# Optimization experiments

Hardware: AMD Instinct MI355X
Metric: run time of the kernel (lower is better)

Reference implementation:

```python
import jax, jax.numpy as jnp
from jax import lax
import numpy as np

B, N, C, P = 8, 512, 256, 7
CQ = C // 4
NMS_THRESH = 0.5
BBOX_XFORM_CLIP = 4.135166556742356  # log(1000/16)


def setup_inputs():
    key = jax.random.key(0)
    ks = jax.random.split(key, 24)
    rn = lambda k, s, sc=0.02: jax.random.normal(k, s, jnp.float32) * sc
    box_feats_q = jax.random.normal(ks[0], (B, N, C, P, P), jnp.float32)
    box_feats_s = jax.random.normal(ks[1], (B, 1, C, P, P), jnp.float32)
    xy = jax.random.uniform(ks[2], (B, N, 2), jnp.float32, 0.0, 700.0)
    wh = jax.random.uniform(ks[3], (B, N, 2), jnp.float32, 8.0, 96.0)
    proposals = jnp.concatenate([xy, xy + wh], axis=-1)  # [B,N,4] valid x1y1x2y2
    image_size = jnp.array([800, 800], jnp.int32)  # (H, W)
    return {
        'box_feats_q': box_feats_q, 'box_feats_s': box_feats_s,
        'proposals': proposals, 'image_size': image_size,
        'W1': rn(ks[4], (CQ, 2 * C)),          # conv1 1x1: 2C -> C/4
        'W2': rn(ks[5], (CQ, CQ, 3, 3)),       # conv2 3x3 valid
        'W3': rn(ks[6], (C, CQ)),              # conv3 1x1: C/4 -> C
        'Wcor': rn(ks[7], (C, C)),             # conv_cor 1x1
        'fc1_w': rn(ks[8], (C, 2 * C)), 'fc1_b': jnp.zeros((C,), jnp.float32),
        'fc2_w': rn(ks[9], (C, C)), 'fc2_b': jnp.zeros((C,), jnp.float32),
        'sfc_w': rn(ks[10], (1, C)), 'sfc_b': jnp.zeros((1,), jnp.float32),
        'scor_w': rn(ks[11], (1, C)), 'scor_b': jnp.zeros((1,), jnp.float32),
        'spr_w': rn(ks[12], (1, C)), 'spr_b': jnp.zeros((1,), jnp.float32),
        'dpr_w': rn(ks[13], (4, C)), 'dpr_b': jnp.zeros((4,), jnp.float32),
    }


def avgpool3(x):  # AvgPool2d(3, stride=1), NCHW
    s = lax.reduce_window(x, 0.0, lax.add, (1, 1, 3, 3), (1, 1, 1, 1), 'VALID')
    return s / 9.0


def head_forward(box_feats_q, box_feats_s, W1, W2, W3, Wcor, fc1_w, fc1_b, fc2_w,
                 fc2_b, sfc_w, sfc_b, scor_w, scor_b, spr_w, spr_b, dpr_w, dpr_b):
    M = B * N
    x_q = box_feats_q.reshape(M, C, P, P)
    x_s = jnp.broadcast_to(box_feats_s, (B, N, C, P, P)).reshape(M, C, P, P)
    # FC branch (avgpool_fc == global mean over 7x7)
    x_fc = jnp.concatenate([x_q.mean((2, 3)), x_s.mean((2, 3))], axis=1)  # [M,2C]
    h = jax.nn.relu(x_fc @ fc1_w.T + fc1_b)
    h = jax.nn.relu(h @ fc2_w.T + fc2_b)
    score_fc = h @ sfc_w.T + sfc_b  # [M,1]
    # Correlation branch: grouped 7x7 conv == per-channel spatial dot product
    x_cor_q = jnp.einsum('oc,mchw->mohw', Wcor, x_q)
    x_cor_s = jnp.einsum('oc,mchw->mohw', Wcor, x_s)
    x_relu = jax.nn.relu((x_cor_q * x_cor_s).sum((2, 3)))  # [M,C]
    score_cor = x_relu @ scor_w.T + scor_b  # [M,1]
    # Conv branch
    x = jnp.concatenate([x_q, x_s], axis=1)                    # [M,2C,7,7]
    x = jax.nn.relu(jnp.einsum('oc,mchw->mohw', W1, x))        # [M,CQ,7,7]
    x = avgpool3(x)                                            # [M,CQ,5,5]
    x = jax.nn.relu(lax.conv_general_dilated(x, W2, (1, 1), 'VALID',
        dimension_numbers=('NCHW', 'OIHW', 'NCHW')))           # [M,CQ,3,3]
    x = jax.nn.relu(jnp.einsum('oc,mchw->mohw', W3, x))        # [M,C,3,3]
    x = avgpool3(x).squeeze(3).squeeze(2)                      # [M,C]
    score_pr = x @ spr_w.T + spr_b
    pred_scores = score_pr + score_cor + score_fc              # [M,1]
    pred_deltas = x @ dpr_w.T + dpr_b                          # [M,4]
    return pred_scores, pred_deltas


def decode_boxes(deltas, boxes):
    w = boxes[:, 2] - boxes[:, 0]
    h = boxes[:, 3] - boxes[:, 1]
    cx = boxes[:, 0] + 0.5 * w
    cy = boxes[:, 1] + 0.5 * h
    dx, dy = deltas[:, 0], deltas[:, 1]
    dw = jnp.minimum(deltas[:, 2], BBOX_XFORM_CLIP)
    dh = jnp.minimum(deltas[:, 3], BBOX_XFORM_CLIP)
    pcx, pcy = dx * w + cx, dy * h + cy
    pw, ph = jnp.exp(dw) * w, jnp.exp(dh) * h
    return jnp.stack([pcx - 0.5 * pw, pcy - 0.5 * ph,
                      pcx + 0.5 * pw, pcy + 0.5 * ph], axis=1)


def nms_mask(boxes, scores, thresh):  # fixed-shape NMS -> keep mask [n]
    n = boxes.shape[0]
    order = jnp.argsort(-scores)
    b = boxes[order]
    area = jnp.maximum(b[:, 2] - b[:, 0], 0) * jnp.maximum(b[:, 3] - b[:, 1], 0)
    idx = jnp.arange(n)

    def body(i, keep):
        x1 = jnp.maximum(b[i, 0], b[:, 0]); y1 = jnp.maximum(b[i, 1], b[:, 1])
        x2 = jnp.minimum(b[i, 2], b[:, 2]); y2 = jnp.minimum(b[i, 3], b[:, 3])
        inter = jnp.maximum(x2 - x1, 0) * jnp.maximum(y2 - y1, 0)
        iou = inter / jnp.maximum(area[i] + area - inter, 1e-9)
        suppress = (iou > thresh) & (idx > i) & keep[i]
        return keep & ~suppress

    keep_sorted = lax.fori_loop(0, n, body, jnp.ones((n,), bool))
    return jnp.zeros((n,), bool).at[order].set(keep_sorted)


def reference(box_feats_q, box_feats_s, proposals, image_size, W1, W2, W3, Wcor,
              fc1_w, fc1_b, fc2_w, fc2_b, sfc_w, sfc_b, scor_w, scor_b,
              spr_w, spr_b, dpr_w, dpr_b):
    pred_scores, pred_deltas = head_forward(
        box_feats_q, box_feats_s, W1, W2, W3, Wcor, fc1_w, fc1_b, fc2_w, fc2_b,
        sfc_w, sfc_b, scor_w, scor_b, spr_w, spr_b, dpr_w, dpr_b)
    M = B * N
    # decode on detached deltas
    pred_boxes = decode_boxes(lax.stop_gradient(pred_deltas), proposals.reshape(M, 4))
    H = image_size[0].astype(jnp.float32)
    W_ = image_size[1].astype(jnp.float32)
    pred_boxes = jnp.stack([
        jnp.clip(pred_boxes[:, 0], 0.0, W_), jnp.clip(pred_boxes[:, 1], 0.0, H),
        jnp.clip(pred_boxes[:, 2], 0.0, W_), jnp.clip(pred_boxes[:, 3], 0.0, H)],
        axis=1).reshape(B, N, 4)
    scores = jax.nn.sigmoid(lax.stop_gradient(pred_scores)).reshape(B, N)
    keep = jax.vmap(lambda bx, sc: nms_mask(bx, sc, NMS_THRESH))(pred_boxes, scores)
    # boxes/scores padded to fixed [B,N,...]; keep mask marks NMS survivors
    return pred_boxes, scores, keep
```

## Files before the change

### kernel.cpp

```cpp
#include <hip/hip_runtime.h>
#include <math.h>

typedef float f4 __attribute__((ext_vector_type(4)));
typedef f4 f4u __attribute__((aligned(4)));
typedef float f32x4 __attribute__((ext_vector_type(4)));
typedef short short8 __attribute__((ext_vector_type(8)));

constexpr int NB  = 8;
constexpr int NN  = 512;
constexpr int NC  = 256;
constexpr int NHW = 49;
constexpr int NM  = NB * NN;
constexpr int XS  = 260;

constexpr size_t WS_SMEAN = 0;
constexpr size_t WS_YST   = 2048;
constexpr size_t WS_UST   = 102400;
constexpr size_t WS_WFH   = 127488;
constexpr size_t WS_WFL   = 168448;
constexpr size_t WS_SP    = 209408;
constexpr size_t WS_QMEAN = 213504;
constexpr size_t WS_SBOX  = WS_QMEAN;
constexpr size_t WS_SAREA = WS_SBOX + 16384;
constexpr size_t WS_SIDX  = WS_SAREA + 4096;
constexpr size_t WS_MASK  = WS_SIDX + 4096;

constexpr size_t OUT_SCORES = (size_t)NM * 4;
constexpr size_t OUT_KEEP   = OUT_SCORES + NM;

__device__ __forceinline__ float block_reduce_sum(float v, float* red) {
    int t = threadIdx.x;
#pragma unroll
    for (int off = 32; off > 0; off >>= 1) v += __shfl_down(v, off, 64);
    __syncthreads();
    if ((t & 63) == 0) red[t >> 6] = v;
    __syncthreads();
    return red[0] + red[1] + red[2] + red[3];
}

__device__ __forceinline__ unsigned short bf16_rne(float f) {
    unsigned u = __float_as_uint(f);
    return (unsigned short)((u + 0x7FFFu + ((u >> 16) & 1u)) >> 16);
}
__device__ __forceinline__ float bf16_to_f(unsigned short h) {
    return __uint_as_float(((unsigned)h) << 16);
}

__device__ __forceinline__ void stage_xT(const float* __restrict__ g, float* sx, int t) {
#pragma unroll
    for (int rep = 0; rep < 13; ++rep) {
        int id = rep * 256 + t;
        if (id < 3136) {
            int c4 = id / 49;
            int hw = id - c4 * 49;
            f4 v;
            v[0] = g[(c4 * 4 + 0) * 49 + hw];
            v[1] = g[(c4 * 4 + 1) * 49 + hw];
            v[2] = g[(c4 * 4 + 2) * 49 + hw];
            v[3] = g[(c4 * 4 + 3) * 49 + hw];
            *(f4*)&sx[hw * XS + c4 * 4] = v;
        }
    }
}

__global__ __launch_bounds__(64) void k_wfrag(
    const float* __restrict__ Wcor, const float* __restrict__ W1,
    float* __restrict__ ws)
{
    int l = threadIdx.x, blk = blockIdx.x;
    int mt = blk >> 3, ks = blk & 7;
    int row = mt * 16 + (l & 15);
    int k0 = ks * 32 + (l >> 4) * 8;
    const float* src = (row < 256) ? (Wcor + (size_t)row * 256 + k0)
                                   : (W1 + (size_t)(row - 256) * 512 + k0);
    short hv[8], lv[8];
#pragma unroll
    for (int j = 0; j < 8; ++j) {
        float v = src[j];
        unsigned short hh = bf16_rne(v);
        unsigned short hl = bf16_rne(v - bf16_to_f(hh));
        hv[j] = (short)hh; lv[j] = (short)hl;
    }
    short* dh = (short*)(ws + WS_WFH) + ((size_t)blk * 64 + l) * 8;
    short* dl = (short*)(ws + WS_WFL) + ((size_t)blk * 64 + l) * 8;
#pragma unroll
    for (int j = 0; j < 8; ++j) { dh[j] = hv[j]; dl[j] = lv[j]; }
}

__global__ __launch_bounds__(256, 2) void k_prep(
    const float* __restrict__ bfs, const float* __restrict__ Wcor,
    const float* __restrict__ W1, float* __restrict__ ws)
{
    __shared__ __align__(16) float smem[49 * XS + 16];
    float* sx = smem;
    int t = threadIdx.x;
    int b = blockIdx.x >> 2;
    int oq = blockIdx.x & 3;

    stage_xT(bfs + (size_t)b * 12544, sx, t);
    __syncthreads();

    if (oq == 0) {
        float s = 0.f;
        for (int hw = 0; hw < 49; ++hw) s += sx[hw * XS + t];
        ws[WS_SMEAN + (size_t)b * 256 + t] = s * (1.f / 49.f);
    }

    int og2 = t >> 3, hwg = t & 7;
    int hwb = (hwg == 7) ? 0 : hwg * 7;
    int oA = oq * 64 + og2 * 2;

    float acc0[7] = {0,0,0,0,0,0,0}, acc1[7] = {0,0,0,0,0,0,0};
    float a1a[7]  = {0,0,0,0,0,0,0}, a1b[7]  = {0,0,0,0,0,0,0};
    const float* xrow = sx + hwb * XS;
    const float* w0r = Wcor + (size_t)oA * 256;
    const float* w1r = Wcor + (size_t)(oA + 1) * 256;
    const float* war = W1 + (size_t)og2 * 512 + 256;
    const float* wbr = W1 + (size_t)(og2 + 32) * 512 + 256;

#pragma unroll 1
    for (int c4 = 0; c4 < 64; ++c4) {
        f4 xv[7];
#pragma unroll
        for (int i = 0; i < 7; ++i) xv[i] = *(const f4*)&xrow[i * XS + c4 * 4];
        f4 w0 = *(const f4*)&w0r[c4 * 4];
        f4 w1 = *(const f4*)&w1r[c4 * 4];
        f4 wa = *(const f4*)&war[c4 * 4];
        f4 wb = *(const f4*)&wbr[c4 * 4];
#pragma unroll
        for (int j = 0; j < 4; ++j) {
#pragma unroll
            for (int i = 0; i < 7; ++i) {
                float x = xv[i][j];
                acc0[i] = fmaf(w0[j], x, acc0[i]);
                acc1[i] = fmaf(w1[j], x, acc1[i]);
                a1a[i]  = fmaf(wa[j], x, a1a[i]);
                a1b[i]  = fmaf(wb[j], x, a1b[i]);
            }
        }
    }

    if (hwg < 7) {
#pragma unroll
        for (int i = 0; i < 7; ++i) {
            int hw = hwb + i;
            ws[WS_YST + ((size_t)b * 256 + oA)     * 49 + hw] = acc0[i];
            ws[WS_YST + ((size_t)b * 256 + oA + 1) * 49 + hw] = acc1[i];
            if (oq == 0) {
                ws[WS_UST + ((size_t)b * 64 + og2)      * 49 + hw] = a1a[i];
                ws[WS_UST + ((size_t)b * 64 + og2 + 32) * 49 + hw] = a1b[i];
            }
        }
    }
}

__global__ __launch_bounds__(256, 3) void k_heavy(
    const float* __restrict__ bfq,
    const float* __restrict__ W2, const float* __restrict__ W3,
    const float* __restrict__ scor_w, const float* __restrict__ scor_b,
    const float* __restrict__ spr_w, const float* __restrict__ spr_b,
    const float* __restrict__ dpr_w, const float* __restrict__ dpr_b,
    const float* __restrict__ proposals, const int* __restrict__ image_size,
    float* __restrict__ ws, float* __restrict__ out)
{
    __shared__ __align__(16) short xh[49 * 256];
    __shared__ __align__(16) short xl[49 * 256];
    __shared__ float red[20];

    int t = threadIdx.x, m = blockIdx.x, b = m >> 9;
    const float* xg = bfq + (size_t)m * 12544 + (size_t)t * 49;

    {
        float qs = 0.f;
#pragma unroll
        for (int r = 0; r < 12; ++r) {
            f4u v = *(const f4u*)&xg[r * 4];
#pragma unroll
            for (int j = 0; j < 4; ++j) {
                int hw = r * 4 + j;
                float x = v[j];
                qs += x;
                unsigned short hh = bf16_rne(x);
                int idx = (hw * 256 + t) ^ ((hw & 7) << 3);
                xh[idx] = (short)hh;
                xl[idx] = (short)bf16_rne(x - bf16_to_f(hh));
            }
        }
        float x48 = xg[48];
        qs += x48;
        unsigned short hh48 = bf16_rne(x48);
        xh[48 * 256 + t] = (short)hh48;
        xl[48 * 256 + t] = (short)bf16_rne(x48 - bf16_to_f(hh48));
        ws[WS_QMEAN + (size_t)m * 256 + t] = qs * (1.f / 49.f);
    }
    __syncthreads();

    int w = t >> 6, l = t & 63, cl = l & 15, g = l >> 4;

    f32x4 acc[5][4];
#pragma unroll
    for (int i = 0; i < 5; ++i)
#pragma unroll
        for (int nt = 0; nt < 4; ++nt) acc[i][nt] = (f32x4)0.f;

    const short* wfH = (const short*)(ws + WS_WFH);
    const short* wfL = (const short*)(ws + WS_WFL);

    int bcol[4];
#pragma unroll
    for (int nt = 0; nt < 4; ++nt) {
        int col = nt * 16 + cl;
        if (col >= 49) col = 0;
        bcol[nt] = col;
    }

#pragma unroll 1
    for (int ks = 0; ks < 8; ++ks) {
        short8 bh[4], bl[4];
#pragma unroll
        for (int nt = 0; nt < 4; ++nt) {
            int col = bcol[nt];
            int idx = (col * 256 + ks * 32 + g * 8) ^ ((col & 7) << 3);
            bh[nt] = *(const short8*)&xh[idx];
            bl[nt] = *(const short8*)&xl[idx];
        }
#pragma unroll
        for (int i = 0; i < 5; ++i) {
            int mt = w + 4 * i;
            size_t off = ((size_t)(mt * 8 + ks) * 64 + l) * 8;
            short8 ah = *(const short8*)&wfH[off];
            short8 al = *(const short8*)&wfL[off];
            acc[i][0] = __builtin_amdgcn_mfma_f32_16x16x32_bf16(ah, bh[0], acc[i][0], 0, 0, 0);
            acc[i][1] = __builtin_amdgcn_mfma_f32_16x16x32_bf16(ah, bh[1], acc[i][1], 0, 0, 0);
            acc[i][2] = __builtin_amdgcn_mfma_f32_16x16x32_bf16(ah, bh[2], acc[i][2], 0, 0, 0);
            acc[i][3] = __builtin_amdgcn_mfma_f32_16x16x32_bf16(ah, bh[3], acc[i][3], 0, 0, 0);
            acc[i][0] = __builtin_amdgcn_mfma_f32_16x16x32_bf16(ah, bl[0], acc[i][0], 0, 0, 0);
            acc[i][1] = __builtin_amdgcn_mfma_f32_16x16x32_bf16(ah, bl[1], acc[i][1], 0, 0, 0);
            acc[i][2] = __builtin_amdgcn_mfma_f32_16x16x32_bf16(ah, bl[2], acc[i][2], 0, 0, 0);
            acc[i][3] = __builtin_amdgcn_mfma_f32_16x16x32_bf16(ah, bl[3], acc[i][3], 0, 0, 0);
            acc[i][0] = __builtin_amdgcn_mfma_f32_16x16x32_bf16(al, bh[0], acc[i][0], 0, 0, 0);
            acc[i][1] = __builtin_amdgcn_mfma_f32_16x16x32_bf16(al, bh[1], acc[i][1], 0, 0, 0);
            acc[i][2] = __builtin_amdgcn_mfma_f32_16x16x32_bf16(al, bh[2], acc[i][2], 0, 0, 0);
            acc[i][3] = __builtin_amdgcn_mfma_f32_16x16x32_bf16(al, bh[3], acc[i][3], 0, 0, 0);
        }
    }

    float csum = 0.f;
    {
        const float* yb = ws + WS_YST + (size_t)b * 256 * 49;
#pragma unroll
        for (int i = 0; i < 4; ++i) {
            int row0 = (w + 4 * i) * 16 + g * 4;
#pragma unroll
            for (int q = 0; q < 4; ++q) {
                int row = row0 + q;
                float p = 0.f;
#pragma unroll
                for (int nt = 0; nt < 4; ++nt) {
                    int col = nt * 16 + cl;
                    if (col < 49) p += acc[i][nt][q] * yb[(size_t)row * 49 + col];
                }
                p += __shfl_xor(p, 1, 64);
                p += __shfl_xor(p, 2, 64);
                p += __shfl_xor(p, 4, 64);
                p += __shfl_xor(p, 8, 64);
                if (cl == 0) csum += fmaxf(p, 0.f) * scor_w[row];
            }
        }
    }
    __syncthreads();

    float* s1    = (float*)xh;
    float* sp1   = s1 + 64 * 52;
    float* cpart = (float*)xl;
    float* sc2T  = cpart + 2816;
    {
        const float* ub = ws + WS_UST + (size_t)b * 64 * 49;
        int ch0 = w * 16 + g * 4;
#pragma unroll
        for (int q = 0; q < 4; ++q) {
            int ch = ch0 + q;
#pragma unroll
            for (int nt = 0; nt < 4; ++nt) {
                int col = nt * 16 + cl;
                if (col < 49)
                    s1[ch * 52 + col] = fmaxf(acc[4][nt][q] + ub[(size_t)ch * 49 + col], 0.f);
            }
        }
    }
    __syncthreads();

    for (int i = t; i < 64 * 25; i += 256) {
        int ch = i / 25, pos = i - ch * 25;
        int py = pos / 5, px = pos - py * 5;
        const float* base = s1 + ch * 52 + py * 7 + px;
        float s = base[0] + base[1] + base[2]
                + base[7] + base[8] + base[9]
                + base[14] + base[15] + base[16];
        sp1[ch * 28 + pos] = s * (1.f / 9.f);
    }
    __syncthreads();

    {
        int oc = t & 63, icq = t >> 6;
        float a9[9] = {0,0,0,0,0,0,0,0,0};
        const float* wb2 = W2 + (size_t)oc * 576 + icq * 16 * 9;
#pragma unroll 1
        for (int ic16 = 0; ic16 < 16; ++ic16) {
            int ic = icq * 16 + ic16;
            const f4* ar = (const f4*)(sp1 + ic * 28);
            float av[28];
            *(f4*)&av[0]  = ar[0];
            *(f4*)&av[4]  = ar[1];
            *(f4*)&av[8]  = ar[2];
            *(f4*)&av[12] = ar[3];
            *(f4*)&av[16] = ar[4];
            *(f4*)&av[20] = ar[5];
            *(f4*)&av[24] = ar[6];
            const float* wi = wb2 + ic16 * 9;
            f4u w0 = *(const f4u*)wi;
            f4u w1 = *(const f4u*)(wi + 4);
            float wv[9] = { w0[0], w0[1], w0[2], w0[3], w1[0], w1[1], w1[2], w1[3], wi[8] };
#pragma unroll
            for (int py = 0; py < 3; ++py)
#pragma unroll
                for (int px = 0; px < 3; ++px) {
                    int p9 = py * 3 + px;
#pragma unroll
                    for (int ky = 0; ky < 3; ++ky)
#pragma unroll
                        for (int kx = 0; kx < 3; ++kx)
                            a9[p9] = fmaf(wv[ky * 3 + kx],
                                          av[(py + ky) * 5 + (px + kx)], a9[p9]);
                }
        }
#pragma unroll
        for (int p = 0; p < 9; ++p)
            cpart[((size_t)icq * 64 + oc) * 11 + p] = a9[p];
    }
    __syncthreads();

    for (int i = t; i < 576; i += 256) {
        int pos = i >> 6, occ = i & 63;
        float s = cpart[((size_t)0 * 64 + occ) * 11 + pos]
                + cpart[((size_t)1 * 64 + occ) * 11 + pos]
                + cpart[((size_t)2 * 64 + occ) * 11 + pos]
                + cpart[((size_t)3 * 64 + occ) * 11 + pos];
        sc2T[pos * 64 + occ] = fmaxf(s, 0.f);
    }
    __syncthreads();

    float xfin;
    {
        float xw[9] = {0,0,0,0,0,0,0,0,0};
        const f4* wr = (const f4*)(W3 + (size_t)t * 64);
#pragma unroll 1
        for (int gg = 0; gg < 16; ++gg) {
            f4 wv4 = wr[gg];
#pragma unroll
            for (int p = 0; p < 9; ++p) {
                f4 c = *(const f4*)(sc2T + p * 64 + gg * 4);
                xw[p] = fmaf(wv4[0], c[0], xw[p]);
                xw[p] = fmaf(wv4[1], c[1], xw[p]);
                xw[p] = fmaf(wv4[2], c[2], xw[p]);
                xw[p] = fmaf(wv4[3], c[3], xw[p]);
            }
        }
        float s = 0.f;
#pragma unroll
        for (int p = 0; p < 9; ++p) s += fmaxf(xw[p], 0.f);
        xfin = s * (1.f / 9.f);
    }

    float v0 = xfin * spr_w[t] + csum;
    float v1 = xfin * dpr_w[0 * 256 + t];
    float v2 = xfin * dpr_w[1 * 256 + t];
    float v3 = xfin * dpr_w[2 * 256 + t];
    float v4 = xfin * dpr_w[3 * 256 + t];
#pragma unroll
    for (int off = 32; off > 0; off >>= 1) {
        v0 += __shfl_xor(v0, off, 64);
        v1 += __shfl_xor(v1, off, 64);
        v2 += __shfl_xor(v2, off, 64);
        v3 += __shfl_xor(v3, off, 64);
        v4 += __shfl_xor(v4, off, 64);
    }
    if (l == 0) {
        red[w * 5 + 0] = v0; red[w * 5 + 1] = v1; red[w * 5 + 2] = v2;
        red[w * 5 + 3] = v3; red[w * 5 + 4] = v4;
    }
    __syncthreads();

    if (t == 0) {
        float r_s  = red[0] + red[5] + red[10] + red[15];
        float r_d0 = red[1] + red[6] + red[11] + red[16];
        float r_d1 = red[2] + red[7] + red[12] + red[17];
        float r_d2 = red[3] + red[8] + red[13] + red[18];
        float r_d3 = red[4] + red[9] + red[14] + red[19];

        ws[WS_SP + m] = r_s + spr_b[0] + scor_b[0];

        float d0 = r_d0 + dpr_b[0];
        float d1 = r_d1 + dpr_b[1];
        float d2 = fminf(r_d2 + dpr_b[2], 4.135166556742356f);
        float d3 = fminf(r_d3 + dpr_b[3], 4.135166556742356f);

        const float* pr = proposals + (size_t)m * 4;
        float x1p = pr[0], y1p = pr[1], x2p = pr[2], y2p = pr[3];
        float wd = x2p - x1p, hd = y2p - y1p;
        float cx = x1p + 0.5f * wd, cy = y1p + 0.5f * hd;
        float pcx = d0 * wd + cx, pcy = d1 * hd + cy;
        float pw = expf(d2) * wd, ph = expf(d3) * hd;
        float Wf = (float)image_size[1];
        float Hf = (float)image_size[0];
        out[(size_t)m * 4 + 0] = fminf(fmaxf(pcx - 0.5f * pw, 0.f), Wf);
        out[(size_t)m * 4 + 1] = fminf(fmaxf(pcy - 0.5f * ph, 0.f), Hf);
        out[(size_t)m * 4 + 2] = fminf(fmaxf(pcx + 0.5f * pw, 0.f), Wf);
        out[(size_t)m * 4 + 3] = fminf(fmaxf(pcy + 0.5f * ph, 0.f), Hf);
    }
}

__global__ __launch_bounds__(256) void k_fc(
    const float* __restrict__ fc1_w, const float* __restrict__ fc1_b,
    const float* __restrict__ fc2_w, const float* __restrict__ fc2_b,
    const float* __restrict__ sfc_w, const float* __restrict__ sfc_b,
    float* __restrict__ ws, float* __restrict__ out)
{
    __shared__ __align__(16) float sxfc[8][512];
    __shared__ __align__(16) float sh1[8][256];
    __shared__ float s_red[8];
    int t = threadIdx.x;
    int m0 = blockIdx.x * 8;

#pragma unroll
    for (int mi = 0; mi < 8; ++mi) {
        int mg = m0 + mi;
        int b = mg >> 9;
        sxfc[mi][t]       = ws[WS_QMEAN + (size_t)mg * 256 + t];
        sxfc[mi][256 + t] = ws[WS_SMEAN + (size_t)b * 256 + t];
    }
    __syncthreads();

    {
        const f4* wr = (const f4*)(fc1_w + t * 512);
        float acc[8] = {0,0,0,0,0,0,0,0};
        for (int k4 = 0; k4 < 128; ++k4) {
            f4 w = wr[k4];
#pragma unroll
            for (int mi = 0; mi < 8; ++mi) {
                f4 x = ((const f4*)sxfc[mi])[k4];
                acc[mi] = fmaf(w[0], x[0], acc[mi]);
                acc[mi] = fmaf(w[1], x[1], acc[mi]);
                acc[mi] = fmaf(w[2], x[2], acc[mi]);
                acc[mi] = fmaf(w[3], x[3], acc[mi]);
            }
        }
        float bb = fc1_b[t];
#pragma unroll
        for (int mi = 0; mi < 8; ++mi) sh1[mi][t] = fmaxf(acc[mi] + bb, 0.f);
    }
    __syncthreads();

    float val[8];
    {
        const f4* wr = (const f4*)(fc2_w + t * 256);
        float acc[8] = {0,0,0,0,0,0,0,0};
        for (int k4 = 0; k4 < 64; ++k4) {
            f4 w = wr[k4];
#pragma unroll
            for (int mi = 0; mi < 8; ++mi) {
                f4 x = ((const f4*)sh1[mi])[k4];
                acc[mi] = fmaf(w[0], x[0], acc[mi]);
                acc[mi] = fmaf(w[1], x[1], acc[mi]);
                acc[mi] = fmaf(w[2], x[2], acc[mi]);
                acc[mi] = fmaf(w[3], x[3], acc[mi]);
            }
        }
        float bb = fc2_b[t];
        float sw = sfc_w[t];
#pragma unroll
        for (int mi = 0; mi < 8; ++mi) val[mi] = sw * fmaxf(acc[mi] + bb, 0.f);
    }

#pragma unroll
    for (int mi = 0; mi < 8; ++mi) {
        float r = block_reduce_sum(val[mi], s_red);
        if (t == 0) {
            float tot = ws[WS_SP + m0 + mi] + (r + sfc_b[0]);
            out[OUT_SCORES + m0 + mi] = 1.0f / (1.0f + expf(-tot));
        }
    }
}

__global__ __launch_bounds__(256) void k_sort(
    const float* __restrict__ out, float* __restrict__ ws)
{
    __shared__ float ssc[512];
    int t = threadIdx.x, b = blockIdx.x;
    const float* sc_g = out + OUT_SCORES + (size_t)b * 512;
    ssc[t] = sc_g[t];
    ssc[t + 256] = sc_g[t + 256];
    __syncthreads();

#pragma unroll
    for (int ii = 0; ii < 2; ++ii) {
        int i = t + ii * 256;
        float si = ssc[i];
        int r = 0;
        for (int j = 0; j < 512; ++j) {
            float sj = ssc[j];
            r += (int)((sj > si) || (sj == si && j < i));
        }
        f4 v = *(const f4*)(out + ((size_t)b * 512 + i) * 4);
        *(f4*)&ws[WS_SBOX + ((size_t)b * 512 + r) * 4] = v;
        ws[WS_SAREA + (size_t)b * 512 + r] =
            fmaxf(v[2] - v[0], 0.f) * fmaxf(v[3] - v[1], 0.f);
        ((int*)ws)[WS_SIDX + (size_t)b * 512 + r] = i;
    }
}

__global__ __launch_bounds__(256) void k_mask(float* __restrict__ ws)
{
    int t = threadIdx.x;
    int wv = t >> 6, lane = t & 63;
    int gi = blockIdx.x * 4 + wv;
    int b = gi >> 9, i = gi & 511;

    f4 bi = *(const f4*)&ws[WS_SBOX + ((size_t)b * 512 + i) * 4];
    float ai = ws[WS_SAREA + (size_t)b * 512 + i];
    unsigned long long* mask = (unsigned long long*)(ws + WS_MASK);

#pragma unroll
    for (int w = 0; w < 8; ++w) {
        int j = w * 64 + lane;
        f4 bj = *(const f4*)&ws[WS_SBOX + ((size_t)b * 512 + j) * 4];
        float aj = ws[WS_SAREA + (size_t)b * 512 + j];
        float xx1 = fmaxf(bi[0], bj[0]), yy1 = fmaxf(bi[1], bj[1]);
        float xx2 = fminf(bi[2], bj[2]), yy2 = fminf(bi[3], bj[3]);
        float inter = fmaxf(xx2 - xx1, 0.f) * fmaxf(yy2 - yy1, 0.f);
        float iou = inter / fmaxf(ai + aj - inter, 1e-9f);
        bool sup = (iou > 0.5f) && (j > i);
        unsigned long long bal = __ballot(sup);
        if (lane == 0) mask[((size_t)b * 512 + i) * 8 + w] = bal;
    }
}

__global__ __launch_bounds__(64) void k_final(
    float* __restrict__ out, const float* __restrict__ wsf)
{
    int lane = threadIdx.x, b = blockIdx.x;
    const unsigned long long* mask =
        (const unsigned long long*)(wsf + WS_MASK) + (size_t)b * 512 * 8;

    unsigned long long kw = ~0ull;
    unsigned long long nxt = (lane < 8) ? mask[lane] : 0ull;

    for (int i = 0; i < 512; ++i) {
        unsigned long long cur = nxt;
        if (i < 511 && lane < 8) nxt = mask[(size_t)(i + 1) * 8 + lane];
        unsigned long long wi = __shfl(kw, i >> 6, 64);
        if ((wi >> (i & 63)) & 1ull) {
            if (lane < 8) kw &= ~cur;
        }
    }

    const int* sidx = ((const int*)wsf) + WS_SIDX + (size_t)b * 512;
#pragma unroll
    for (int w = 0; w < 8; ++w) {
        unsigned long long word = __shfl(kw, w, 64);
        int r = w * 64 + lane;
        out[OUT_KEEP + (size_t)b * 512 + sidx[r]] =
            ((word >> lane) & 1ull) ? 1.0f : 0.0f;
    }
}

extern "C" void kernel_launch(void* const* d_in, const int* in_sizes, int n_in,
                              void* d_out, int out_size, void* d_ws, size_t ws_size,
                              hipStream_t stream) {
    const float* bfq       = (const float*)d_in[0];
    const float* bfs       = (const float*)d_in[1];
    const float* proposals = (const float*)d_in[2];
    const int*   image_sz  = (const int*)d_in[3];
    const float* W1        = (const float*)d_in[4];
    const float* W2        = (const float*)d_in[5];
    const float* W3        = (const float*)d_in[6];
    const float* Wcor      = (const float*)d_in[7];
    const float* fc1_w     = (const float*)d_in[8];
    const float* fc1_b     = (const float*)d_in[9];
    const float* fc2_w     = (const float*)d_in[10];
    const float* fc2_b     = (const float*)d_in[11];
    const float* sfc_w     = (const float*)d_in[12];
    const float* sfc_b     = (const float*)d_in[13];
    const float* scor_w    = (const float*)d_in[14];
    const float* scor_b    = (const float*)d_in[15];
    const float* spr_w     = (const float*)d_in[16];
    const float* spr_b     = (const float*)d_in[17];
    const float* dpr_w     = (const float*)d_in[18];
    const float* dpr_b     = (const float*)d_in[19];
    float* out = (float*)d_out;
    float* ws  = (float*)d_ws;

    k_wfrag<<<160, 64, 0, stream>>>(Wcor, W1, ws);
    k_prep<<<32, 256, 0, stream>>>(bfs, Wcor, W1, ws);
    k_heavy<<<NM, 256, 0, stream>>>(bfq, W2, W3,
                                    scor_w, scor_b, spr_w, spr_b,
                                    dpr_w, dpr_b, proposals, image_sz, ws, out);
    k_fc<<<NM / 8, 256, 0, stream>>>(fc1_w, fc1_b, fc2_w, fc2_b,
                                     sfc_w, sfc_b, ws, out);
    k_sort<<<NB, 256, 0, stream>>>(out, ws);
    k_mask<<<1024, 256, 0, stream>>>(ws);
    k_final<<<NB, 64, 0, stream>>>(out, ws);
}
```

Baseline: 504.8 us.

## Stage input features in two channel halves to halve LDS and raise occupancy

The k_heavy kernel no longer stages all 256 channels of the 7x7 ROI as bf16 hi/lo into shared memory at once. It now stages 128 channels at a time and runs the MFMA k-loop per half, with both halves reusing one float buffer. This roughly halves the per-block LDS footprint, and launch bounds are raised from 3 to 4 blocks per CU. The cost is extra __syncthreads barriers between staging and compute, serialized load/compute phases, and tighter register limits that could cause spills.

```diff
diff --git a/kernel.cpp b/kernel.cpp
--- a/kernel.cpp
+++ b/kernel.cpp
@@ -154,7 +154,7 @@
     }
 }
 
-__global__ __launch_bounds__(256, 3) void k_heavy(
+__global__ __launch_bounds__(256, 4) void k_heavy(
     const float* __restrict__ bfq,
     const float* __restrict__ W2, const float* __restrict__ W3,
     const float* __restrict__ scor_w, const float* __restrict__ scor_b,
@@ -163,39 +163,16 @@
     const float* __restrict__ proposals, const int* __restrict__ image_size,
     float* __restrict__ ws, float* __restrict__ out)
 {
-    __shared__ __align__(16) short xh[49 * 256];
-    __shared__ __align__(16) short xl[49 * 256];
+    __shared__ __align__(16) float smem[6272];
+    __shared__ float qpart[2][256];
     __shared__ float red[20];
 
+    short* xh = (short*)smem;
+    short* xl = ((short*)smem) + 6272;
+
     int t = threadIdx.x, m = blockIdx.x, b = m >> 9;
-    const float* xg = bfq + (size_t)m * 12544 + (size_t)t * 49;
-
-    {
-        float qs = 0.f;
-#pragma unroll
-        for (int r = 0; r < 12; ++r) {
-            f4u v = *(const f4u*)&xg[r * 4];
-#pragma unroll
-            for (int j = 0; j < 4; ++j) {
-                int hw = r * 4 + j;
-                float x = v[j];
-                qs += x;
-                unsigned short hh = bf16_rne(x);
-                int idx = (hw * 256 + t) ^ ((hw & 7) << 3);
-                xh[idx] = (short)hh;
-                xl[idx] = (short)bf16_rne(x - bf16_to_f(hh));
-            }
-        }
-        float x48 = xg[48];
-        qs += x48;
-        unsigned short hh48 = bf16_rne(x48);
-        xh[48 * 256 + t] = (short)hh48;
-        xl[48 * 256 + t] = (short)bf16_rne(x48 - bf16_to_f(hh48));
-        ws[WS_QMEAN + (size_t)m * 256 + t] = qs * (1.f / 49.f);
-    }
-    __syncthreads();
-
     int w = t >> 6, l = t & 63, cl = l & 15, g = l >> 4;
+    int c = t & 127, part = t >> 7;
 
     f32x4 acc[5][4];
 #pragma unroll
@@ -214,36 +191,78 @@
         bcol[nt] = col;
     }
 
+    auto stage_half = [&](int half) {
+        const float* xs = bfq + (size_t)m * 12544
+                        + (size_t)(half * 128 + c) * 49 + part * 25;
+        float qs = 0.f;
+#pragma unroll
+        for (int r = 0; r < 6; ++r) {
+            f4u v = *(const f4u*)&xs[r * 4];
+#pragma unroll
+            for (int j = 0; j < 4; ++j) {
+                int hw = part * 25 + r * 4 + j;
+                float x = v[j];
+                qs += x;
+                unsigned short hh = bf16_rne(x);
+                int idx = (hw * 128 + c) ^ ((hw & 7) << 3);
+                xh[idx] = (short)hh;
+                xl[idx] = (short)bf16_rne(x - bf16_to_f(hh));
+            }
+        }
+        if (part == 0) {
+            float x = xs[24];
+            qs += x;
+            unsigned short hh = bf16_rne(x);
+            int idx = (24 * 128 + c);
+            xh[idx] = (short)hh;
+            xl[idx] = (short)bf16_rne(x - bf16_to_f(hh));
+        }
+        qpart[part][half * 128 + c] = qs;
+    };
+
+    auto kloop = [&](int half) {
 #pragma unroll 1
-    for (int ks = 0; ks < 8; ++ks) {
-        short8 bh[4], bl[4];
-#pragma unroll
-        for (int nt = 0; nt < 4; ++nt) {
-            int col = bcol[nt];
-            int idx = (col * 256 + ks * 32 + g * 8) ^ ((col & 7) << 3);
-            bh[nt] = *(const short8*)&xh[idx];
-            bl[nt] = *(const short8*)&xl[idx];
-        }
-#pragma unroll
-        for (int i = 0; i < 5; ++i) {
-            int mt = w + 4 * i;
-            size_t off = ((size_t)(mt * 8 + ks) * 64 + l) * 8;
-            short8 ah = *(const short8*)&wfH[off];
-            short8 al = *(const short8*)&wfL[off];
-            acc[i][0] = __builtin_amdgcn_mfma_f32_16x16x32_bf16(ah, bh[0], acc[i][0], 0, 0, 0);
-            acc[i][1] = __builtin_amdgcn_mfma_f32_16x16x32_bf16(ah, bh[1], acc[i][1], 0, 0, 0);
-            acc[i][2] = __builtin_amdgcn_mfma_f32_16x16x32_bf16(ah, bh[2], acc[i][2], 0, 0, 0);
-            acc[i][3] = __builtin_amdgcn_mfma_f32_16x16x32_bf16(ah, bh[3], acc[i][3], 0, 0, 0);
-            acc[i][0] = __builtin_amdgcn_mfma_f32_16x16x32_bf16(ah, bl[0], acc[i][0], 0, 0, 0);
-            acc[i][1] = __builtin_amdgcn_mfma_f32_16x16x32_bf16(ah, bl[1], acc[i][1], 0, 0, 0);
-            acc[i][2] = __builtin_amdgcn_mfma_f32_16x16x32_bf16(ah, bl[2], acc[i][2], 0, 0, 0);
-            acc[i][3] = __builtin_amdgcn_mfma_f32_16x16x32_bf16(ah, bl[3], acc[i][3], 0, 0, 0);
-            acc[i][0] = __builtin_amdgcn_mfma_f32_16x16x32_bf16(al, bh[0], acc[i][0], 0, 0, 0);
-            acc[i][1] = __builtin_amdgcn_mfma_f32_16x16x32_bf16(al, bh[1], acc[i][1], 0, 0, 0);
-            acc[i][2] = __builtin_amdgcn_mfma_f32_16x16x32_bf16(al, bh[2], acc[i][2], 0, 0, 0);
-            acc[i][3] = __builtin_amdgcn_mfma_f32_16x16x32_bf16(al, bh[3], acc[i][3], 0, 0, 0);
-        }
-    }
+        for (int ksl = 0; ksl < 4; ++ksl) {
+            int ks = half * 4 + ksl;
+            short8 bh[4], bl[4];
+#pragma unroll
+            for (int nt = 0; nt < 4; ++nt) {
+                int col = bcol[nt];
+                int idx = (col * 128 + ksl * 32 + g * 8) ^ ((col & 7) << 3);
+                bh[nt] = *(const short8*)&xh[idx];
+                bl[nt] = *(const short8*)&xl[idx];
+            }
+#pragma unroll
+            for (int i = 0; i < 5; ++i) {
+                int mt = w + 4 * i;
+                size_t off = ((size_t)(mt * 8 + ks) * 64 + l) * 8;
+                short8 ah = *(const short8*)&wfH[off];
+                short8 al = *(const short8*)&wfL[off];
+                acc[i][0] = __builtin_amdgcn_mfma_f32_16x16x32_bf16(ah, bh[0], acc[i][0], 0, 0, 0);
+                acc[i][1] = __builtin_amdgcn_mfma_f32_16x16x32_bf16(ah, bh[1], acc[i][1], 0, 0, 0);
+                acc[i][2] = __builtin_amdgcn_mfma_f32_16x16x32_bf16(ah, bh[2], acc[i][2], 0, 0, 0);
+                acc[i][3] = __builtin_amdgcn_mfma_f32_16x16x32_bf16(ah, bh[3], acc[i][3], 0, 0, 0);
+                acc[i][0] = __builtin_amdgcn_mfma_f32_16x16x32_bf16(ah, bl[0], acc[i][0], 0, 0, 0);
+                acc[i][1] = __builtin_amdgcn_mfma_f32_16x16x32_bf16(ah, bl[1], acc[i][1], 0, 0, 0);
+                acc[i][2] = __builtin_amdgcn_mfma_f32_16x16x32_bf16(ah, bl[2], acc[i][2], 0, 0, 0);
+                acc[i][3] = __builtin_amdgcn_mfma_f32_16x16x32_bf16(ah, bl[3], acc[i][3], 0, 0, 0);
+                acc[i][0] = __builtin_amdgcn_mfma_f32_16x16x32_bf16(al, bh[0], acc[i][0], 0, 0, 0);
+                acc[i][1] = __builtin_amdgcn_mfma_f32_16x16x32_bf16(al, bh[1], acc[i][1], 0, 0, 0);
+                acc[i][2] = __builtin_amdgcn_mfma_f32_16x16x32_bf16(al, bh[2], acc[i][2], 0, 0, 0);
+                acc[i][3] = __builtin_amdgcn_mfma_f32_16x16x32_bf16(al, bh[3], acc[i][3], 0, 0, 0);
+            }
+        }
+    };
+
+    stage_half(0);
+    __syncthreads();
+    kloop(0);
+    __syncthreads();
+    stage_half(1);
+    __syncthreads();
+    ws[WS_QMEAN + (size_t)m * 256 + t] =
+        (qpart[0][t] + qpart[1][t]) * (1.f / 49.f);
+    kloop(1);
 
     float csum = 0.f;
     {
@@ -270,10 +289,11 @@
     }
     __syncthreads();
 
-    float* s1    = (float*)xh;
-    float* sp1   = s1 + 64 * 52;
-    float* cpart = (float*)xl;
-    float* sc2T  = cpart + 2816;
+    float* s1    = smem;
+    float* sp1   = smem + 3328;
+    float* cpart = smem;
+    float* sc2T  = smem + 3328;
+
     {
         const float* ub = ws + WS_UST + (size_t)b * 64 * 49;
         int ch0 = w * 16 + g * 4;
@@ -334,6 +354,7 @@
                                           av[(py + ky) * 5 + (px + kx)], a9[p9]);
                 }
         }
+        __syncthreads();
 #pragma unroll
         for (int p = 0; p < 9; ++p)
             cpart[((size_t)icq * 64 + oc) * 11 + p] = a9[p];
@@ -359,11 +380,11 @@
             f4 wv4 = wr[gg];
 #pragma unroll
             for (int p = 0; p < 9; ++p) {
-                f4 c = *(const f4*)(sc2T + p * 64 + gg * 4);
-                xw[p] = fmaf(wv4[0], c[0], xw[p]);
-                xw[p] = fmaf(wv4[1], c[1], xw[p]);
-                xw[p] = fmaf(wv4[2], c[2], xw[p]);
-                xw[p] = fmaf(wv4[3], c[3], xw[p]);
+                f4 cc = *(const f4*)(sc2T + p * 64 + gg * 4);
+                xw[p] = fmaf(wv4[0], cc[0], xw[p]);
+                xw[p] = fmaf(wv4[1], cc[1], xw[p]);
+                xw[p] = fmaf(wv4[2], cc[2], xw[p]);
+                xw[p] = fmaf(wv4[3], cc[3], xw[p]);
             }
         }
         float s = 0.f;
```

Result: slower. 581.1 us (+15.1%).
